# Performance work log

Hardware: AMD Instinct MI355X
Metric: run time of the kernel (lower is better)

The kernel has to match this reference:

```python
import jax, jax.numpy as jnp
import numpy as np

N_HEADS, D_MODEL, D_HEAD = 16, 1024, 64
BATCH, SEQ = 2, 2048
INIT_STD = 0.02
MASK_FILL = -100000.0  # module uses -1e5, not -inf


def setup_inputs() -> dict:
    key = jax.random.key(0)
    ks = jax.random.split(key, 5)
    x = jax.random.normal(ks[0], (BATCH, SEQ, D_MODEL), dtype=jnp.float32)
    W_Q = INIT_STD * jax.random.normal(ks[1], (N_HEADS, D_MODEL, D_HEAD), dtype=jnp.float32)
    W_K = INIT_STD * jax.random.normal(ks[2], (N_HEADS, D_MODEL, D_HEAD), dtype=jnp.float32)
    W_V = INIT_STD * jax.random.normal(ks[3], (N_HEADS, D_MODEL, D_HEAD), dtype=jnp.float32)
    W_O = INIT_STD * jax.random.normal(ks[4], (N_HEADS, D_HEAD, D_MODEL), dtype=jnp.float32)
    b_Q = jnp.zeros((N_HEADS, D_HEAD), dtype=jnp.float32)
    b_K = jnp.zeros((N_HEADS, D_HEAD), dtype=jnp.float32)
    b_V = jnp.zeros((N_HEADS, D_HEAD), dtype=jnp.float32)
    b_O = jnp.zeros((D_MODEL,), dtype=jnp.float32)
    return {"normalized_resid_pre": x, "W_Q": W_Q, "W_K": W_K, "W_V": W_V,
            "W_O": W_O, "b_Q": b_Q, "b_K": b_K, "b_V": b_V, "b_O": b_O}


def reference(normalized_resid_pre, W_Q, W_K, W_V, W_O, b_Q, b_K, b_V, b_O):
    x = normalized_resid_pre  # [b, s, d_model]
    Q = jnp.einsum('bpd,hde->bphe', x, W_Q) + b_Q  # [b, s, h, dh]
    K = jnp.einsum('bpd,hde->bphe', x, W_K) + b_K
    V = jnp.einsum('bpd,hde->bphe', x, W_V) + b_V
    scale = 1.0 / jnp.sqrt(jnp.float32(D_HEAD))
    scores = jnp.einsum('bqhe,bkhe->bhqk', Q, K) * scale  # [b, h, q, k]
    s = scores.shape[-1]
    causal = jnp.triu(jnp.ones((s, s), dtype=bool), k=1)  # True above diagonal
    scores = jnp.where(causal, jnp.float32(MASK_FILL), scores)
    attn = jax.nn.softmax(scores, axis=-1)
    Z = jnp.einsum('bkhe,bhqk->bqhe', V, attn)  # [b, q, h, dh]
    out = jnp.einsum('bqhe,hed->bqd', Z, W_O) + b_O  # [b, q, d_model]
    return out
```

## Files before the change

kernel.cpp:

```cpp
#include <hip/hip_runtime.h>
#include <math.h>

#define BATCH 2
#define SEQ   2048
#define NH    16
#define DH    64
#define DM    1024

typedef __attribute__((ext_vector_type(8))) short bf16x8;
typedef __attribute__((ext_vector_type(8))) unsigned short u16x8;
typedef __attribute__((ext_vector_type(4))) float f32x4;

__device__ __forceinline__ unsigned short f2bf(float f) {
    union { float f; unsigned u; } v; v.f = f;
    unsigned r = v.u + 0x7FFF + ((v.u >> 16) & 1);
    return (unsigned short)(r >> 16);
}
__device__ __forceinline__ unsigned short f2bf_fast(float f) {
    union { float f; unsigned u; } v; v.f = f;
    return (unsigned short)((v.u + 0x8000u) >> 16);
}

__device__ __forceinline__ void gl2lds16(const void* g, void* l) {
    __builtin_amdgcn_global_load_lds(
        (const __attribute__((address_space(1))) void*)g,
        (__attribute__((address_space(3))) void*)l,
        16, 0, 0);
}

__global__ __launch_bounds__(256) void conv_fused(
    const float* __restrict__ x,
    const float* __restrict__ WQ, const float* __restrict__ WK,
    const float* __restrict__ WV, const float* __restrict__ WO,
    unsigned short* __restrict__ xb,
    unsigned short* __restrict__ Wt, unsigned short* __restrict__ WOt)
{
    __shared__ float sT[64][68];
    const int tid = threadIdx.x;

    if (blockIdx.x < 2048) {
        size_t idx = ((size_t)blockIdx.x * 256 + tid) * 8;
        float4 a = *(const float4*)(x + idx);
        float4 b = *(const float4*)(x + idx + 4);
        u16x8 o;
        o[0] = f2bf(a.x); o[1] = f2bf(a.y); o[2] = f2bf(a.z); o[3] = f2bf(a.w);
        o[4] = f2bf(b.x); o[5] = f2bf(b.y); o[6] = f2bf(b.z); o[7] = f2bf(b.w);
        *(u16x8*)(xb + idx) = o;
        return;
    }
    const int t = blockIdx.x - 2048;
    if (t < 768) {
        int m = t >> 8, rem = t & 255, h = rem >> 4, dblk = rem & 15;
        const float* W = (m == 0) ? WQ : (m == 1) ? WK : WV;
        const float* in = W + (size_t)h * 65536 + dblk * 4096;
#pragma unroll
        for (int it = 0; it < 4; it++) {
            int idx = it * 1024 + tid * 4;
            int r = idx >> 6, c = idx & 63;
            *(float4*)(&sT[r][c]) = *(const float4*)(&in[(size_t)r * 64 + c]);
        }
        __syncthreads();
        unsigned short* out = Wt + (size_t)m * 1048576 + (size_t)h * 65536 + dblk * 64;
#pragma unroll
        for (int it = 0; it < 4; it++) {
            int idx = it * 1024 + tid * 4;
            int e = idx >> 6, d0 = idx & 63;
            ushort4 o;
            unsigned short* op = (unsigned short*)&o;
#pragma unroll
            for (int j = 0; j < 4; j++) op[j] = f2bf(sT[d0 + j][e]);
            *(ushort4*)&out[(size_t)e * 1024 + d0] = o;
        }
    } else {
        int tt = t - 768, rblk = tt >> 4, cblk = tt & 15;
        const float* in = WO + (size_t)rblk * 64 * 1024 + cblk * 64;
#pragma unroll
        for (int it = 0; it < 4; it++) {
            int idx = it * 1024 + tid * 4;
            int r = idx >> 6, c = idx & 63;
            *(float4*)(&sT[r][c]) = *(const float4*)(&in[(size_t)r * 1024 + c]);
        }
        __syncthreads();
        unsigned short* out = WOt + (size_t)cblk * 64 * 1024 + rblk * 64;
#pragma unroll
        for (int it = 0; it < 4; it++) {
            int idx = it * 1024 + tid * 4;
            int d = idx >> 6, he0 = idx & 63;
            ushort4 o;
            unsigned short* op = (unsigned short*)&o;
#pragma unroll
            for (int j = 0; j < 4; j++) op[j] = f2bf(sT[he0 + j][d]);
            *(ushort4*)&out[(size_t)d * 1024 + he0] = o;
        }
    }
}

__global__ __launch_bounds__(256) void qkv_mfma(
    const unsigned short* __restrict__ xb,
    const unsigned short* __restrict__ Wt,
    const float* __restrict__ bQ, const float* __restrict__ bK,
    const float* __restrict__ bV,
    unsigned short* __restrict__ Q, unsigned short* __restrict__ K,
    unsigned short* __restrict__ Vt)
{
    __shared__ __align__(16) unsigned short sA[128 * 64];
    __shared__ __align__(16) unsigned short sB[128 * 64];

    const int rowTile = blockIdx.x;
    const int m  = blockIdx.y >> 3;
    const int hp = blockIdx.y & 7;
    const unsigned short* Wm = Wt + (size_t)m * 1048576 + (size_t)hp * 2 * 65536;

    const int tid  = threadIdx.x;
    const int w    = tid >> 6;
    const int lane = tid & 63;
    const int l15  = lane & 15;
    const int quad = lane >> 4;
    const int rw   = (w & 1) * 64;
    const int cw   = (w >> 1) * 64;
    const int rowBase = rowTile * 128;

    const int crow = lane >> 3;
    const int ccs  = (((lane & 7) ^ crow) * 8);

    f32x4 acc[4][4];
#pragma unroll
    for (int i = 0; i < 4; i++)
#pragma unroll
        for (int j = 0; j < 4; j++) acc[i][j] = (f32x4){0.f, 0.f, 0.f, 0.f};

    for (int k0 = 0; k0 < DM; k0 += 64) {
        __syncthreads();
#pragma unroll
        for (int c = 0; c < 4; c++) {
            const int chunk = w * 4 + c;
            const int rr = chunk * 8 + crow;
            gl2lds16(&xb[(size_t)(rowBase + rr) * DM + k0 + ccs], &sA[chunk * 512]);
            gl2lds16(&Wm[(size_t)rr * DM + k0 + ccs],             &sB[chunk * 512]);
        }
        __syncthreads();

#pragma unroll
        for (int ks = 0; ks < 2; ks++) {
            bf16x8 af[4], bf[4];
#pragma unroll
            for (int i = 0; i < 4; i++) {
                int ar = rw + i * 16 + l15;
                af[i] = *(const bf16x8*)&sA[ar * 64 + (((ks * 4 + quad) ^ (ar & 7)) * 8)];
            }
#pragma unroll
            for (int j = 0; j < 4; j++) {
                int br = cw + j * 16 + l15;
                bf[j] = *(const bf16x8*)&sB[br * 64 + (((ks * 4 + quad) ^ (br & 7)) * 8)];
            }
            if (m == 2) {
#pragma unroll
                for (int i = 0; i < 4; i++)
#pragma unroll
                    for (int j = 0; j < 4; j++)
                        acc[i][j] = __builtin_amdgcn_mfma_f32_16x16x32_bf16(
                            af[i], bf[j], acc[i][j], 0, 0, 0);
            } else {
#pragma unroll
                for (int i = 0; i < 4; i++)
#pragma unroll
                    for (int j = 0; j < 4; j++)
                        acc[i][j] = __builtin_amdgcn_mfma_f32_16x16x32_bf16(
                            bf[j], af[i], acc[i][j], 0, 0, 0);
            }
        }
    }

    if (m == 2) {
#pragma unroll
        for (int j = 0; j < 4; j++) {
            int col = cw + j * 16 + l15;
            int h = hp * 2 + (col >> 6);
            int e = col & 63;
            float bv = bV[h * DH + e];
#pragma unroll
            for (int i = 0; i < 4; i++) {
                int row0 = rowBase + rw + i * 16 + quad * 4;
                int b = row0 >> 11, s0 = row0 & 2047;
                ushort4 o;
                unsigned short* op = (unsigned short*)&o;
#pragma unroll
                for (int r = 0; r < 4; r++) op[r] = f2bf(acc[i][j][r] + bv);
                *(ushort4*)&Vt[(((size_t)b * NH + h) * DH + e) * SEQ + s0] = o;
            }
        }
    } else {
        const float* bias = (m == 0) ? bQ : bK;
        unsigned short* Out = (m == 0) ? Q : K;
        const float scale = (m == 0) ? 0.125f : 1.0f;
#pragma unroll
        for (int i = 0; i < 4; i++) {
            int row = rowBase + rw + i * 16 + l15;
            int b = row >> 11, s = row & 2047;
#pragma unroll
            for (int j = 0; j < 4; j++) {
                int col0 = cw + j * 16 + quad * 4;
                int h = hp * 2 + (col0 >> 6);
                int e0 = col0 & 63;
                ushort4 o;
                unsigned short* op = (unsigned short*)&o;
#pragma unroll
                for (int r = 0; r < 4; r++)
                    op[r] = f2bf((acc[i][j][r] + bias[h * DH + e0 + r]) * scale);
                *(ushort4*)&Out[(((size_t)b * NH + h) * SEQ + s) * DH + e0] = o;
            }
        }
    }
}

__global__ __launch_bounds__(256) void attn_mfma(
    const unsigned short* __restrict__ Q,
    const unsigned short* __restrict__ K,
    const unsigned short* __restrict__ Vt,
    unsigned short* __restrict__ Z)
{
    __shared__ __align__(16) unsigned short sK [64 * 64];
    __shared__ __align__(16) unsigned short sV [64 * 64];
    __shared__ __align__(16) unsigned short sPA[64 * 72];
    __shared__ __align__(16) unsigned short sPB[64 * 72];

    const int h   = blockIdx.x & 15;
    const int b   = (blockIdx.x >> 4) & 1;
    const int i   = blockIdx.x >> 5;
    const int qtA = i;
    const int qtB = 31 - i;

    const int tid  = threadIdx.x;
    const int w    = tid >> 6;
    const int lane = tid & 63;
    const int l15  = lane & 15;
    const int quad = lane >> 4;

    const size_t headOff = ((size_t)b * NH + h) * SEQ * DH;
    const unsigned short* Qh  = Q  + headOff;
    const unsigned short* Kh  = K  + headOff;
    const unsigned short* Vth = Vt + headOff;

    const unsigned short* qrowA =
        Qh + (size_t)(qtA * 64 + w * 16 + l15) * DH + quad * 8;
    const unsigned short* qrowB =
        Qh + (size_t)(qtB * 64 + w * 16 + l15) * DH + quad * 8;
    bf16x8 qA[2], qB[2];
    qA[0] = *(const bf16x8*)(qrowA);  qA[1] = *(const bf16x8*)(qrowA + 32);
    qB[0] = *(const bf16x8*)(qrowB);  qB[1] = *(const bf16x8*)(qrowB + 32);

    f32x4 OA[4], OB[4];
#pragma unroll
    for (int s = 0; s < 4; s++) {
        OA[s] = (f32x4){0.f, 0.f, 0.f, 0.f};
        OB[s] = (f32x4){0.f, 0.f, 0.f, 0.f};
    }
    float lAa = 0.f, lBa = 0.f;

    const int crow = lane >> 3;
    const int ccs  = (((lane & 7) ^ crow) * 8);

    for (int kt = 0; kt <= qtB; kt++) {
        const int k0 = kt * 64;
        __syncthreads();
#pragma unroll
        for (int c = 0; c < 2; c++) {
            const int chunk = w * 2 + c;
            const int rr = chunk * 8 + crow;
            gl2lds16(&Kh[(size_t)(k0 + rr) * DH + ccs], &sK[chunk * 512]);
            gl2lds16(&Vth[(size_t)rr * SEQ + k0 + ccs], &sV[chunk * 512]);
        }
        __syncthreads();

        bf16x8 kf[8], vf[8];
#pragma unroll
        for (int ks = 0; ks < 2; ks++)
#pragma unroll
            for (int sub = 0; sub < 4; sub++) {
                int rr = sub * 16 + l15;
                int sw = ((ks * 4 + quad) ^ (rr & 7)) * 8;
                kf[ks * 4 + sub] = *(const bf16x8*)&sK[rr * 64 + sw];
                vf[ks * 4 + sub] = *(const bf16x8*)&sV[rr * 64 + sw];
            }

        const bool doA = (kt <= qtA);

        f32x4 SB[4];
#pragma unroll
        for (int s = 0; s < 4; s++) SB[s] = (f32x4){0.f, 0.f, 0.f, 0.f};
#pragma unroll
        for (int ks = 0; ks < 2; ks++)
#pragma unroll
            for (int sub = 0; sub < 4; sub++)
                SB[sub] = __builtin_amdgcn_mfma_f32_16x16x32_bf16(
                    kf[ks * 4 + sub], qB[ks], SB[sub], 0, 0, 0);
        f32x4 SA[4];
        if (doA) {
#pragma unroll
            for (int s = 0; s < 4; s++) SA[s] = (f32x4){0.f, 0.f, 0.f, 0.f};
#pragma unroll
            for (int ks = 0; ks < 2; ks++)
#pragma unroll
                for (int sub = 0; sub < 4; sub++)
                    SA[sub] = __builtin_amdgcn_mfma_f32_16x16x32_bf16(
                        kf[ks * 4 + sub], qA[ks], SA[sub], 0, 0, 0);
        }

        const bool diagB = (kt == qtB);
#pragma unroll
        for (int sub = 0; sub < 4; sub++) {
            ushort4 o;
            unsigned short* op = (unsigned short*)&o;
#pragma unroll
            for (int r = 0; r < 4; r++) {
                float pb = __expf(SB[sub][r]);
                if (diagB && (sub * 16 + quad * 4 + r > w * 16 + l15)) pb = 0.f;
                lBa += pb;
                op[r] = f2bf_fast(pb);
            }
            *(ushort4*)&sPB[(w * 16 + l15) * 72 + sub * 16 + quad * 4] = o;
        }
        if (doA) {
            const bool diagA = (kt == qtA);
#pragma unroll
            for (int sub = 0; sub < 4; sub++) {
                ushort4 o;
                unsigned short* op = (unsigned short*)&o;
#pragma unroll
                for (int r = 0; r < 4; r++) {
                    float pa = __expf(SA[sub][r]);
                    if (diagA && (sub * 16 + quad * 4 + r > w * 16 + l15)) pa = 0.f;
                    lAa += pa;
                    op[r] = f2bf_fast(pa);
                }
                *(ushort4*)&sPA[(w * 16 + l15) * 72 + sub * 16 + quad * 4] = o;
            }
        }
        __builtin_amdgcn_wave_barrier();

#pragma unroll
        for (int ks = 0; ks < 2; ks++) {
            bf16x8 pb = *(const bf16x8*)
                &sPB[(w * 16 + l15) * 72 + ks * 32 + quad * 8];
#pragma unroll
            for (int sub = 0; sub < 4; sub++)
                OB[sub] = __builtin_amdgcn_mfma_f32_16x16x32_bf16(
                    vf[ks * 4 + sub], pb, OB[sub], 0, 0, 0);
        }
        if (doA) {
#pragma unroll
            for (int ks = 0; ks < 2; ks++) {
                bf16x8 pa = *(const bf16x8*)
                    &sPA[(w * 16 + l15) * 72 + ks * 32 + quad * 8];
#pragma unroll
                for (int sub = 0; sub < 4; sub++)
                    OA[sub] = __builtin_amdgcn_mfma_f32_16x16x32_bf16(
                        vf[ks * 4 + sub], pa, OA[sub], 0, 0, 0);
            }
        }
        __builtin_amdgcn_wave_barrier();
    }

    lAa += __shfl_xor(lAa, 16, 64);
    lAa += __shfl_xor(lAa, 32, 64);
    lBa += __shfl_xor(lBa, 16, 64);
    lBa += __shfl_xor(lBa, 32, 64);
    const float rlA = 1.0f / lAa;
    const float rlB = 1.0f / lBa;

#pragma unroll
    for (int half = 0; half < 2; half++) {
        const int qt = half ? qtB : qtA;
        const f32x4* O4 = half ? OB : OA;
        const float rl = half ? rlB : rlA;
        const int q = qt * 64 + w * 16 + l15;
        unsigned short* zrow = Z + ((size_t)b * SEQ + q) * DM + h * DH;
#pragma unroll
        for (int sub = 0; sub < 4; sub++) {
            ushort4 o;
            unsigned short* op = (unsigned short*)&o;
#pragma unroll
            for (int r = 0; r < 4; r++) op[r] = f2bf(O4[sub][r] * rl);
            *(ushort4*)&zrow[sub * 16 + quad * 4] = o;
        }
    }
}

__global__ __launch_bounds__(256) void out_mfma(
    const unsigned short* __restrict__ Zb,
    const unsigned short* __restrict__ WOt,
    const float* __restrict__ bO,
    float* __restrict__ out)
{
    __shared__ __align__(16) unsigned short sA[64 * 64];
    __shared__ __align__(16) unsigned short sB[128 * 64];

    const int rowTile = blockIdx.x;
    const int colTile = blockIdx.y;
    const int rowBase = rowTile * 64;
    const int colBase = colTile * 128;

    const int tid  = threadIdx.x;
    const int w    = tid >> 6;
    const int lane = tid & 63;
    const int l15  = lane & 15;
    const int quad = lane >> 4;
    const int rw   = (w & 1) * 32;
    const int cw   = (w >> 1) * 64;

    const int crow = lane >> 3;
    const int ccs  = (((lane & 7) ^ crow) * 8);

    f32x4 acc[2][4];
#pragma unroll
    for (int i = 0; i < 2; i++)
#pragma unroll
        for (int j = 0; j < 4; j++) acc[i][j] = (f32x4){0.f, 0.f, 0.f, 0.f};

    for (int k0 = 0; k0 < DM; k0 += 64) {
        __syncthreads();
#pragma unroll
        for (int c = 0; c < 2; c++) {
            const int chunk = w * 2 + c;
            const int rr = chunk * 8 + crow;
            gl2lds16(&Zb[(size_t)(rowBase + rr) * DM + k0 + ccs], &sA[chunk * 512]);
        }
#pragma unroll
        for (int c = 0; c < 4; c++) {
            const int chunk = w * 4 + c;
            const int rr = chunk * 8 + crow;
            gl2lds16(&WOt[(size_t)(colBase + rr) * DM + k0 + ccs], &sB[chunk * 512]);
        }
        __syncthreads();

#pragma unroll
        for (int ks = 0; ks < 2; ks++) {
            bf16x8 af[2], bf[4];
#pragma unroll
            for (int i = 0; i < 2; i++) {
                int ar = rw + i * 16 + l15;
                af[i] = *(const bf16x8*)&sA[ar * 64 + (((ks * 4 + quad) ^ (ar & 7)) * 8)];
            }
#pragma unroll
            for (int j = 0; j < 4; j++) {
                int br = cw + j * 16 + l15;
                bf[j] = *(const bf16x8*)&sB[br * 64 + (((ks * 4 + quad) ^ (br & 7)) * 8)];
            }
#pragma unroll
            for (int i = 0; i < 2; i++)
#pragma unroll
                for (int j = 0; j < 4; j++)
                    acc[i][j] = __builtin_amdgcn_mfma_f32_16x16x32_bf16(
                        bf[j], af[i], acc[i][j], 0, 0, 0);
        }
    }

#pragma unroll
    for (int i = 0; i < 2; i++) {
        int row = rowBase + rw + i * 16 + l15;
#pragma unroll
        for (int j = 0; j < 4; j++) {
            int col0 = colBase + cw + j * 16 + quad * 4;
            float4 o;
            o.x = acc[i][j][0] + bO[col0 + 0];
            o.y = acc[i][j][1] + bO[col0 + 1];
            o.z = acc[i][j][2] + bO[col0 + 2];
            o.w = acc[i][j][3] + bO[col0 + 3];
            *(float4*)&out[(size_t)row * DM + col0] = o;
        }
    }
}

extern "C" void kernel_launch(void* const* d_in, const int* in_sizes, int n_in,
                              void* d_out, int out_size, void* d_ws, size_t ws_size,
                              hipStream_t stream)
{
    const float* x  = (const float*)d_in[0];
    const float* WQ = (const float*)d_in[1];
    const float* WK = (const float*)d_in[2];
    const float* WV = (const float*)d_in[3];
    const float* WO = (const float*)d_in[4];
    const float* bQ = (const float*)d_in[5];
    const float* bK = (const float*)d_in[6];
    const float* bV = (const float*)d_in[7];
    const float* bO = (const float*)d_in[8];
    float* out = (float*)d_out;

    const size_t M4 = 4194304;
    unsigned short* xb  = (unsigned short*)d_ws;
    unsigned short* Wt  = xb + M4;
    unsigned short* WOt = Wt + 3 * 1048576;
    unsigned short* Qw  = WOt + 1048576;
    unsigned short* Kw  = Qw + M4;
    unsigned short* Vtw = Kw + M4;
    unsigned short* Zb  = xb;

    conv_fused<<<3072, 256, 0, stream>>>(x, WQ, WK, WV, WO, xb, Wt, WOt);

    dim3 g1(32, 24);
    qkv_mfma<<<g1, 256, 0, stream>>>(xb, Wt, bQ, bK, bV, Qw, Kw, Vtw);

    attn_mfma<<<512, 256, 0, stream>>>(Qw, Kw, Vtw, Zb);

    dim3 g3(64, 8);
    out_mfma<<<g3, 256, 0, stream>>>(Zb, WOt, bO, out);
}
```

Baseline: 201.8 us.

## Double-buffer LDS tiles in QKV, attention and output kernels

Adds a second LDS buffer to the QKV projection, attention and output projection kernels. Each kernel now prefetches the next K-tile with global_load_lds while computing on the current tile, and drops one of the two barriers per iteration. The aim is to hide global-to-LDS load latency behind the MFMA work. It also hoists the Q/K bias loads out of the epilogue loop as float4 reads. The cost is doubled LDS use (64KB in the QKV kernel), which may lower occupancy. Correctness relies on the barrier waiting for the async LDS loads to finish.

```diff
diff --git a/kernel.cpp b/kernel.cpp
--- a/kernel.cpp
+++ b/kernel.cpp
@@ -103,8 +103,8 @@
     unsigned short* __restrict__ Q, unsigned short* __restrict__ K,
     unsigned short* __restrict__ Vt)
 {
-    __shared__ __align__(16) unsigned short sA[128 * 64];
-    __shared__ __align__(16) unsigned short sB[128 * 64];
+    __shared__ __align__(16) unsigned short sA[2][128 * 64];
+    __shared__ __align__(16) unsigned short sB[2][128 * 64];
 
     const int rowTile = blockIdx.x;
     const int m  = blockIdx.y >> 3;
@@ -129,16 +129,30 @@
 #pragma unroll
         for (int j = 0; j < 4; j++) acc[i][j] = (f32x4){0.f, 0.f, 0.f, 0.f};
 
-    for (int k0 = 0; k0 < DM; k0 += 64) {
+#pragma unroll
+    for (int c = 0; c < 4; c++) {
+        const int chunk = w * 4 + c;
+        const int rr = chunk * 8 + crow;
+        gl2lds16(&xb[(size_t)(rowBase + rr) * DM + ccs], &sA[0][chunk * 512]);
+        gl2lds16(&Wm[(size_t)rr * DM + ccs],             &sB[0][chunk * 512]);
+    }
+
+    for (int kt = 0; kt < 16; kt++) {
         __syncthreads();
-#pragma unroll
-        for (int c = 0; c < 4; c++) {
-            const int chunk = w * 4 + c;
-            const int rr = chunk * 8 + crow;
-            gl2lds16(&xb[(size_t)(rowBase + rr) * DM + k0 + ccs], &sA[chunk * 512]);
-            gl2lds16(&Wm[(size_t)rr * DM + k0 + ccs],             &sB[chunk * 512]);
-        }
-        __syncthreads();
+        if (kt < 15) {
+            const int k1 = (kt + 1) * 64;
+            unsigned short* dA = sA[(kt + 1) & 1];
+            unsigned short* dB = sB[(kt + 1) & 1];
+#pragma unroll
+            for (int c = 0; c < 4; c++) {
+                const int chunk = w * 4 + c;
+                const int rr = chunk * 8 + crow;
+                gl2lds16(&xb[(size_t)(rowBase + rr) * DM + k1 + ccs], &dA[chunk * 512]);
+                gl2lds16(&Wm[(size_t)rr * DM + k1 + ccs],             &dB[chunk * 512]);
+            }
+        }
+        const unsigned short* pA = sA[kt & 1];
+        const unsigned short* pB = sB[kt & 1];
 
 #pragma unroll
         for (int ks = 0; ks < 2; ks++) {
@@ -146,12 +160,12 @@
 #pragma unroll
             for (int i = 0; i < 4; i++) {
                 int ar = rw + i * 16 + l15;
-                af[i] = *(const bf16x8*)&sA[ar * 64 + (((ks * 4 + quad) ^ (ar & 7)) * 8)];
+                af[i] = *(const bf16x8*)&pA[ar * 64 + (((ks * 4 + quad) ^ (ar & 7)) * 8)];
             }
 #pragma unroll
             for (int j = 0; j < 4; j++) {
                 int br = cw + j * 16 + l15;
-                bf[j] = *(const bf16x8*)&sB[br * 64 + (((ks * 4 + quad) ^ (br & 7)) * 8)];
+                bf[j] = *(const bf16x8*)&pB[br * 64 + (((ks * 4 + quad) ^ (br & 7)) * 8)];
             }
             if (m == 2) {
 #pragma unroll
@@ -193,21 +207,28 @@
         const float* bias = (m == 0) ? bQ : bK;
         unsigned short* Out = (m == 0) ? Q : K;
         const float scale = (m == 0) ? 0.125f : 1.0f;
+        float4 bb[4];
+        int hj[4], e0j[4];
+#pragma unroll
+        for (int j = 0; j < 4; j++) {
+            int col0 = cw + j * 16 + quad * 4;
+            hj[j] = hp * 2 + (col0 >> 6);
+            e0j[j] = col0 & 63;
+            bb[j] = *(const float4*)&bias[hj[j] * DH + e0j[j]];
+        }
 #pragma unroll
         for (int i = 0; i < 4; i++) {
             int row = rowBase + rw + i * 16 + l15;
             int b = row >> 11, s = row & 2047;
 #pragma unroll
             for (int j = 0; j < 4; j++) {
-                int col0 = cw + j * 16 + quad * 4;
-                int h = hp * 2 + (col0 >> 6);
-                int e0 = col0 & 63;
+                const float* bp = (const float*)&bb[j];
                 ushort4 o;
                 unsigned short* op = (unsigned short*)&o;
 #pragma unroll
                 for (int r = 0; r < 4; r++)
-                    op[r] = f2bf((acc[i][j][r] + bias[h * DH + e0 + r]) * scale);
-                *(ushort4*)&Out[(((size_t)b * NH + h) * SEQ + s) * DH + e0] = o;
+                    op[r] = f2bf((acc[i][j][r] + bp[r]) * scale);
+                *(ushort4*)&Out[(((size_t)b * NH + hj[j]) * SEQ + s) * DH + e0j[j]] = o;
             }
         }
     }
@@ -219,8 +240,8 @@
     const unsigned short* __restrict__ Vt,
     unsigned short* __restrict__ Z)
 {
-    __shared__ __align__(16) unsigned short sK [64 * 64];
-    __shared__ __align__(16) unsigned short sV [64 * 64];
+    __shared__ __align__(16) unsigned short sK [2][64 * 64];
+    __shared__ __align__(16) unsigned short sV [2][64 * 64];
     __shared__ __align__(16) unsigned short sPA[64 * 72];
     __shared__ __align__(16) unsigned short sPB[64 * 72];
 
@@ -260,17 +281,30 @@
     const int crow = lane >> 3;
     const int ccs  = (((lane & 7) ^ crow) * 8);
 
+#pragma unroll
+    for (int c = 0; c < 2; c++) {
+        const int chunk = w * 2 + c;
+        const int rr = chunk * 8 + crow;
+        gl2lds16(&Kh[(size_t)rr * DH + ccs],  &sK[0][chunk * 512]);
+        gl2lds16(&Vth[(size_t)rr * SEQ + ccs], &sV[0][chunk * 512]);
+    }
+
     for (int kt = 0; kt <= qtB; kt++) {
-        const int k0 = kt * 64;
         __syncthreads();
-#pragma unroll
-        for (int c = 0; c < 2; c++) {
-            const int chunk = w * 2 + c;
-            const int rr = chunk * 8 + crow;
-            gl2lds16(&Kh[(size_t)(k0 + rr) * DH + ccs], &sK[chunk * 512]);
-            gl2lds16(&Vth[(size_t)rr * SEQ + k0 + ccs], &sV[chunk * 512]);
-        }
-        __syncthreads();
+        if (kt < qtB) {
+            const int k1 = (kt + 1) * 64;
+            unsigned short* dK = sK[(kt + 1) & 1];
+            unsigned short* dV = sV[(kt + 1) & 1];
+#pragma unroll
+            for (int c = 0; c < 2; c++) {
+                const int chunk = w * 2 + c;
+                const int rr = chunk * 8 + crow;
+                gl2lds16(&Kh[(size_t)(k1 + rr) * DH + ccs], &dK[chunk * 512]);
+                gl2lds16(&Vth[(size_t)rr * SEQ + k1 + ccs], &dV[chunk * 512]);
+            }
+        }
+        const unsigned short* pK = sK[kt & 1];
+        const unsigned short* pV = sV[kt & 1];
 
         bf16x8 kf[8], vf[8];
 #pragma unroll
@@ -279,8 +313,8 @@
             for (int sub = 0; sub < 4; sub++) {
                 int rr = sub * 16 + l15;
                 int sw = ((ks * 4 + quad) ^ (rr & 7)) * 8;
-                kf[ks * 4 + sub] = *(const bf16x8*)&sK[rr * 64 + sw];
-                vf[ks * 4 + sub] = *(const bf16x8*)&sV[rr * 64 + sw];
+                kf[ks * 4 + sub] = *(const bf16x8*)&pK[rr * 64 + sw];
+                vf[ks * 4 + sub] = *(const bf16x8*)&pV[rr * 64 + sw];
             }
 
         const bool doA = (kt <= qtA);
@@ -392,8 +426,8 @@
     const float* __restrict__ bO,
     float* __restrict__ out)
 {
-    __shared__ __align__(16) unsigned short sA[64 * 64];
-    __shared__ __align__(16) unsigned short sB[128 * 64];
+    __shared__ __align__(16) unsigned short sA[2][64 * 64];
+    __shared__ __align__(16) unsigned short sB[2][128 * 64];
 
     const int rowTile = blockIdx.x;
     const int colTile = blockIdx.y;
@@ -417,21 +451,40 @@
 #pragma unroll
         for (int j = 0; j < 4; j++) acc[i][j] = (f32x4){0.f, 0.f, 0.f, 0.f};
 
-    for (int k0 = 0; k0 < DM; k0 += 64) {
+#pragma unroll
+    for (int c = 0; c < 2; c++) {
+        const int chunk = w * 2 + c;
+        const int rr = chunk * 8 + crow;
+        gl2lds16(&Zb[(size_t)(rowBase + rr) * DM + ccs], &sA[0][chunk * 512]);
+    }
+#pragma unroll
+    for (int c = 0; c < 4; c++) {
+        const int chunk = w * 4 + c;
+        const int rr = chunk * 8 + crow;
+        gl2lds16(&WOt[(size_t)(colBase + rr) * DM + ccs], &sB[0][chunk * 512]);
+    }
+
+    for (int kt = 0; kt < 16; kt++) {
         __syncthreads();
-#pragma unroll
-        for (int c = 0; c < 2; c++) {
-            const int chunk = w * 2 + c;
-            const int rr = chunk * 8 + crow;
-            gl2lds16(&Zb[(size_t)(rowBase + rr) * DM + k0 + ccs], &sA[chunk * 512]);
-        }
-#pragma unroll
-        for (int c = 0; c < 4; c++) {
-            const int chunk = w * 4 + c;
-            const int rr = chunk * 8 + crow;
-            gl2lds16(&WOt[(size_t)(colBase + rr) * DM + k0 + ccs], &sB[chunk * 512]);
-        }
-        __syncthreads();
+        if (kt < 15) {
+            const int k1 = (kt + 1) * 64;
+            unsigned short* dA = sA[(kt + 1) & 1];
+            unsigned short* dB = sB[(kt + 1) & 1];
+#pragma unroll
+            for (int c = 0; c < 2; c++) {
+                const int chunk = w * 2 + c;
+                const int rr = chunk * 8 + crow;
+                gl2lds16(&Zb[(size_t)(rowBase + rr) * DM + k1 + ccs], &dA[chunk * 512]);
+            }
+#pragma unroll
+            for (int c = 0; c < 4; c++) {
+                const int chunk = w * 4 + c;
+                const int rr = chunk * 8 + crow;
+                gl2lds16(&WOt[(size_t)(colBase + rr) * DM + k1 + ccs], &dB[chunk * 512]);
+            }
+        }
+        const unsigned short* pA = sA[kt & 1];
+        const unsigned short* pB = sB[kt & 1];
 
 #pragma unroll
         for (int ks = 0; ks < 2; ks++) {
@@ -439,12 +492,12 @@
 #pragma unroll
             for (int i = 0; i < 2; i++) {
                 int ar = rw + i * 16 + l15;
-                af[i] = *(const bf16x8*)&sA[ar * 64 + (((ks * 4 + quad) ^ (ar & 7)) * 8)];
+                af[i] = *(const bf16x8*)&pA[ar * 64 + (((ks * 4 + quad) ^ (ar & 7)) * 8)];
             }
 #pragma unroll
             for (int j = 0; j < 4; j++) {
                 int br = cw + j * 16 + l15;
-                bf[j] = *(const bf16x8*)&sB[br * 64 + (((ks * 4 + quad) ^ (br & 7)) * 8)];
+                bf[j] = *(const bf16x8*)&pB[br * 64 + (((ks * 4 + quad) ^ (br & 7)) * 8)];
             }
 #pragma unroll
             for (int i = 0; i < 2; i++)
```

Result: faster. 186.1 us (-7.8%).
